# Kernel tuning notes

Hardware: AMD Instinct MI355X
Metric: run time of the kernel (lower is better)

Reference implementation:

```python
import jax, jax.numpy as jnp
import numpy as np

B, D, C, P = 1024, 768, 150, 64  # batch, in_feats, num_labels, proj2 dim
POS_M, NEG_M = 0.7, 1.4


def setup_inputs() -> dict:
    key = jax.random.key(0)
    ks = jax.random.split(key, 8)
    return {
        "x": jax.random.normal(ks[0], (B, D), jnp.float32),
        "lb": jax.random.randint(ks[1], (B,), 0, C + 1),
        "mem": jax.random.normal(ks[2], (C, D), jnp.float32),
        "fc_w": jax.random.normal(ks[3], (2 * D, 2 * D), jnp.float32) * 0.02,
        "fc_b": jnp.zeros((2 * D,), jnp.float32),
        "p1_w": jax.random.normal(ks[4], (1, 2 * D), jnp.float32) * 0.02,
        "p1_b": jnp.zeros((1,), jnp.float32),
        "p2_w": jax.random.normal(ks[5], (P, 2 * D), jnp.float32) * 0.02,
        "p2_b": jnp.zeros((P,), jnp.float32),
    }


def reference(x, lb, mem, fc_w, fc_b, p1_w, p1_b, p2_w, p2_b):
    d = x.shape[1]
    # cat([a, b], 1) @ fc_w.T == a @ Wx.T + b @ Wm.T  (exact split of the linear)
    Wx, Wm = fc_w[:, :d], fc_w[:, d:]
    xh = x @ Wx.T + fc_b                                # [B, 2D]

    # --- get_logit ---
    seen_h = jax.nn.relu(xh[:, None, :] + mem @ Wm.T)   # [B, C, 2D]
    seen = jnp.einsum('bce,e->bc', seen_h, p1_w[0]) + p1_b[0]   # [B, C]
    uh = jax.nn.relu(xh)                                # cat([x, zeros]) path
    unseen = uh @ p1_w.T + p1_b                         # [B, 1]
    logits = jnp.concatenate([seen, unseen], axis=1)    # [B, C+1]

    # --- masked log-softmax losses (pos_adapte) ---
    labels = jax.nn.one_hot(lb, C + 1, dtype=jnp.float32)
    th = jnp.zeros_like(labels).at[:, -1].set(1.0)
    labels = labels.at[:, -1].set(0.0)
    p_mask = labels + th
    n_mask = 1.0 - labels
    BIG = 1e30
    loss1 = -(jax.nn.log_softmax(logits - (1.0 - p_mask) * BIG, -1) * labels).sum(1)
    loss2 = -(jax.nn.log_softmax(logits - (1.0 - n_mask) * BIG, -1) * th).sum(1)
    loss_cls = (loss1 + loss2).mean()

    # --- metric loss on unseen embedding ---
    u = uh @ p2_w.T + p2_b                              # [B, 64]
    u = u / jnp.maximum(jnp.linalg.norm(u, axis=1, keepdims=True), 1e-12)
    sq_n = (u * u).sum(1)
    sq = sq_n[:, None] + sq_n[None, :] - 2.0 * (u @ u.T)
    err = sq <= 0.0
    dist = jnp.sqrt(jnp.clip(sq, 1e-16, None)) * (~err).astype(u.dtype)
    same = lb[:, None] == lb[None, :]
    eye = jnp.eye(dist.shape[0], dtype=bool)
    pos = (same & ~eye).astype(dist.dtype)
    neg = (~same).astype(dist.dtype)
    pos_l = (jax.nn.relu(dist - POS_M) * pos).sum() / jnp.maximum(pos.sum(), 1.0)
    neg_l = (jax.nn.relu(NEG_M - dist) * neg).sum() / jnp.maximum(neg.sum(), 1.0)

    return loss_cls + pos_l + neg_l
```

## Files before the change

### kernel.cpp

```cpp
#include <hip/hip_runtime.h>
#include <math.h>

#define B_    1024
#define D_    768
#define C_    150
#define P_    64
#define TWOD  1536
#define NCLS  151
#define CPAD  256

#define ECHUNKS 16
#define ECHUNK  96

#define ASTR  40
#define USTRU 120
#define USTR  72

#define OFF_MH      0
#define OFF_XH      (OFF_MH + (C_ * TWOD) / 2)
#define OFF_PARTIAL (OFF_XH + (B_ * TWOD) / 2)
#define OFF_UHF     (OFF_PARTIAL + ECHUNKS * B_ * CPAD)
#define OFF_SQN     (OFF_UHF + (B_ * P_) / 2)
#define OFF_CLS     (OFF_SQN + B_)
#define OFF_PAIR    (OFF_CLS + B_)
#define OFF_XBF     (OFF_PAIR + 1024)
#define OFF_MEMBF   (OFF_XBF + (B_ * D_) / 2)
#define OFF_WBF     (OFF_MEMBF + (C_ * D_) / 2)
#define OFF_P2H     (OFF_WBF + (TWOD * TWOD) / 2)
#define OFF_P1H     (OFF_P2H + (P_ * TWOD) / 2)

typedef __bf16    bfx8   __attribute__((ext_vector_type(8)));
typedef _Float16  fp16x8 __attribute__((ext_vector_type(8)));
typedef _Float16  h2v    __attribute__((ext_vector_type(2)));
typedef float     f32x4  __attribute__((ext_vector_type(4)));

__device__ inline ushort f2bf(float f) {
    union { float f; unsigned u; } c; c.f = f;
    unsigned r = c.u + 0x7fffu + ((c.u >> 16) & 1u);
    return (ushort)(r >> 16);
}
__device__ inline ushort f2h(float f) {
    _Float16 h = (_Float16)f;
    return __builtin_bit_cast(ushort, h);
}
__device__ inline unsigned addrelu2(unsigned a, unsigned m) {
    h2v s = __builtin_bit_cast(h2v, a) + __builtin_bit_cast(h2v, m);
    h2v z = {(_Float16)0.f, (_Float16)0.f};
    s = __builtin_elementwise_max(s, z);
    return __builtin_bit_cast(unsigned, s);
}
__device__ inline unsigned relu2(unsigned a) {
    h2v s = __builtin_bit_cast(h2v, a);
    h2v z = {(_Float16)0.f, (_Float16)0.f};
    s = __builtin_elementwise_max(s, z);
    return __builtin_bit_cast(unsigned, s);
}
__device__ inline float dot2acc(unsigned a, unsigned b, float c) {
    return __builtin_amdgcn_fdot2(__builtin_bit_cast(h2v, a),
                                  __builtin_bit_cast(h2v, b), c, false);
}

#define X4   (B_ * D_ / 4)
#define MEM4 (C_ * D_ / 4)
#define W4   (TWOD * TWOD / 4)
#define P24  (P_ * TWOD / 4)
#define P14  (TWOD / 4)
#define TOT4 (X4 + MEM4 + W4 + P24 + P14)

__global__ __launch_bounds__(256) void prep_cvt(
    const float* __restrict__ x, const float* __restrict__ mem,
    const float* __restrict__ w, const float* __restrict__ p2w,
    const float* __restrict__ p1w,
    ushort* __restrict__ xb, ushort* __restrict__ memb,
    ushort* __restrict__ wb, ushort* __restrict__ p2h,
    ushort* __restrict__ p1h)
{
    int i = blockIdx.x * 256 + threadIdx.x;
    if (i >= TOT4) return;
    const float* src; ushort* dst; int off; bool bf;
    if (i < X4)                        { src = x;   dst = xb;   off = i; bf = true; }
    else if (i < X4 + MEM4)            { src = mem; dst = memb; off = i - X4; bf = true; }
    else if (i < X4 + MEM4 + W4)       { src = w;   dst = wb;   off = i - X4 - MEM4; bf = true; }
    else if (i < X4 + MEM4 + W4 + P24) { src = p2w; dst = p2h;  off = i - X4 - MEM4 - W4; bf = false; }
    else                               { src = p1w; dst = p1h;  off = i - X4 - MEM4 - W4 - P24; bf = false; }
    float4 v = ((const float4*)src)[off];
    ushort4 o;
    if (bf) { o.x = f2bf(v.x); o.y = f2bf(v.y); o.z = f2bf(v.z); o.w = f2bf(v.w); }
    else    { o.x = f2h(v.x);  o.y = f2h(v.y);  o.z = f2h(v.z);  o.w = f2h(v.w); }
    ((ushort4*)dst)[off] = o;
}

__global__ __launch_bounds__(256) void gemm_all(
    const ushort* __restrict__ xbf, const ushort* __restrict__ membf,
    const ushort* __restrict__ wbf, const float* __restrict__ fc_b,
    ushort* __restrict__ xh, ushort* __restrict__ mh)
{
    __shared__ ushort As[64 * ASTR];
    __shared__ ushort Bs[128 * ASTR];
    const int id = blockIdx.x;
    const int t  = threadIdx.x;

    const ushort* A; ushort* Out; int M, m0, n0, koff; bool xblk;
    if (id < 192) {
        xblk = true;  A = xbf;  Out = xh; M = B_;
        m0 = (id & 15) * 64; n0 = (id >> 4) * 128; koff = 0;
    } else {
        int q = id - 192;
        xblk = false; A = membf; Out = mh; M = C_;
        m0 = (q % 3) * 64; n0 = (q / 3) * 128; koff = D_;
    }

    const int wave = t >> 6, lane = t & 63;
    const int wm = (wave & 1) * 32, wn = (wave >> 1) * 64;
    const int fm = lane & 15, quad = lane >> 4;

    const int row_a = t >> 2, qa = (t & 3) * 8;
    const int ar = min(m0 + row_a, M - 1);
    const ushort* Arow = A + (size_t)ar * D_ + qa;
    const ushort* Brow = wbf + (size_t)(n0 + row_a) * TWOD + koff + qa;

    f32x4 acc[2][4];
#pragma unroll
    for (int j = 0; j < 4; ++j) {
        float bv = xblk ? fc_b[n0 + wn + j * 16 + fm] : 0.f;
#pragma unroll
        for (int i = 0; i < 2; ++i)
            acc[i][j] = (f32x4){bv, bv, bv, bv};
    }

    uint4 pa  = *(const uint4*)(Arow);
    uint4 pb0 = *(const uint4*)(Brow);
    uint4 pb1 = *(const uint4*)(Brow + 64 * TWOD);

    for (int k0 = 0; k0 < D_; k0 += 32) {
        __syncthreads();
        *(uint4*)&As[row_a * ASTR + qa] = pa;
        *(uint4*)&Bs[row_a * ASTR + qa] = pb0;
        *(uint4*)&Bs[(64 + row_a) * ASTR + qa] = pb1;
        __syncthreads();
        if (k0 + 32 < D_) {
            pa  = *(const uint4*)(Arow + k0 + 32);
            pb0 = *(const uint4*)(Brow + k0 + 32);
            pb1 = *(const uint4*)(Brow + 64 * TWOD + k0 + 32);
        }
        bfx8 af[2], bf[4];
#pragma unroll
        for (int i = 0; i < 2; ++i)
            af[i] = *(const bfx8*)&As[(wm + i * 16 + fm) * ASTR + quad * 8];
#pragma unroll
        for (int j = 0; j < 4; ++j)
            bf[j] = *(const bfx8*)&Bs[(wn + j * 16 + fm) * ASTR + quad * 8];
#pragma unroll
        for (int i = 0; i < 2; ++i)
#pragma unroll
            for (int j = 0; j < 4; ++j)
                acc[i][j] = __builtin_amdgcn_mfma_f32_16x16x32_bf16(
                    af[i], bf[j], acc[i][j], 0, 0, 0);
    }

#pragma unroll
    for (int i = 0; i < 2; ++i)
#pragma unroll
        for (int j = 0; j < 4; ++j)
#pragma unroll
            for (int r = 0; r < 4; ++r) {
                int row = m0 + wm + i * 16 + quad * 4 + r;
                int col = n0 + wn + j * 16 + fm;
                if (row < M) Out[(size_t)row * TWOD + col] = f2h(acc[i][j][r]);
            }
}

__global__ __launch_bounds__(256) void fused_tile(
    const ushort* __restrict__ xh, const ushort* __restrict__ mh,
    const ushort* __restrict__ p1h, const ushort* __restrict__ p2h,
    float* __restrict__ partial)
{
    __shared__ __align__(16) char smem[46080];
    const int t  = threadIdx.x;
    const int b0 = blockIdx.x * 128;
    const int z  = blockIdx.z;
    const int e0 = z * ECHUNK;

    if (blockIdx.y == 3) {
        ushort* Au = (ushort*)smem;
        ushort* Wu = (ushort*)(smem + 30720);
        const int wave = t >> 6, lane = t & 63;
        const int fm = lane & 15, quad = lane >> 4;

        {
            const int row = t >> 1, kh = (t & 1) * 48;
            const ushort* src = xh + (size_t)(b0 + row) * TWOD + e0 + kh;
            uint4 v[6];
#pragma unroll
            for (int i = 0; i < 6; ++i) v[i] = *(const uint4*)&src[i * 8];
#pragma unroll
            for (int i = 0; i < 6; ++i) {
                v[i].x = relu2(v[i].x); v[i].y = relu2(v[i].y);
                v[i].z = relu2(v[i].z); v[i].w = relu2(v[i].w);
                *(uint4*)&Au[row * USTRU + kh + i * 8] = v[i];
            }
        }
        {
            const int row = t >> 2, ks = (t & 3) * 24;
            const ushort* pw = p2h + (size_t)row * TWOD + e0 + ks;
#pragma unroll
            for (int i = 0; i < 3; ++i)
                *(uint4*)&Wu[row * USTRU + ks + i * 8] = *(const uint4*)&pw[i * 8];
        }
        __syncthreads();

        f32x4 uacc[2][4];
#pragma unroll
        for (int i = 0; i < 2; ++i)
#pragma unroll
            for (int j = 0; j < 4; ++j) uacc[i][j] = (f32x4){0.f, 0.f, 0.f, 0.f};
#pragma unroll
        for (int k0 = 0; k0 < ECHUNK; k0 += 32) {
            fp16x8 af[2], bf[4];
#pragma unroll
            for (int i = 0; i < 2; ++i)
                af[i] = *(const fp16x8*)&Au[(wave * 32 + i * 16 + fm) * USTRU + k0 + quad * 8];
#pragma unroll
            for (int j = 0; j < 4; ++j)
                bf[j] = *(const fp16x8*)&Wu[(j * 16 + fm) * USTRU + k0 + quad * 8];
#pragma unroll
            for (int i = 0; i < 2; ++i)
#pragma unroll
                for (int j = 0; j < 4; ++j)
                    uacc[i][j] = __builtin_amdgcn_mfma_f32_16x16x32_f16(
                        af[i], bf[j], uacc[i][j], 0, 0, 0);
        }
#pragma unroll
        for (int i = 0; i < 2; ++i)
#pragma unroll
            for (int j = 0; j < 4; ++j)
#pragma unroll
                for (int r = 0; r < 4; ++r) {
                    int row = b0 + wave * 32 + i * 16 + quad * 4 + r;
                    partial[((size_t)z * B_ + row) * CPAD + 192 + j * 16 + fm] =
                        uacc[i][j][r];
                }
        return;
    }

    unsigned* xT = (unsigned*)smem;
    unsigned* mT = (unsigned*)(smem + 24576);
    unsigned* wT = (unsigned*)(smem + 36864);
    const int c0 = blockIdx.y * 64;
    const int tm = t & 15, tn = t >> 4;

    {
        const int row = t >> 1, ph = (t & 1) * 48;
        const ushort* src = xh + (size_t)(b0 + row) * TWOD + e0 + ph;
        uint4 v[6];
#pragma unroll
        for (int i = 0; i < 6; ++i) v[i] = *(const uint4*)&src[i * 8];
#pragma unroll
        for (int i = 0; i < 6; ++i) {
            const int ep = (t & 1) * 24 + i * 4;
            xT[(ep + 0) * 128 + row] = v[i].x;
            xT[(ep + 1) * 128 + row] = v[i].y;
            xT[(ep + 2) * 128 + row] = v[i].z;
            xT[(ep + 3) * 128 + row] = v[i].w;
        }
    }
    {
        const int col = t & 63, seg = t >> 6;
        const int gc  = c0 + col;
        uint4 v[3];
        if (gc < C_) {
            const ushort* src = mh + (size_t)gc * TWOD + e0 + seg * 24;
#pragma unroll
            for (int i = 0; i < 3; ++i) v[i] = *(const uint4*)&src[i * 8];
        } else {
#pragma unroll
            for (int i = 0; i < 3; ++i) v[i] = make_uint4(0, 0, 0, 0);
        }
#pragma unroll
        for (int i = 0; i < 3; ++i) {
            const int ep = seg * 12 + i * 4;
            mT[(ep + 0) * 64 + col] = v[i].x;
            mT[(ep + 1) * 64 + col] = v[i].y;
            mT[(ep + 2) * 64 + col] = v[i].z;
            mT[(ep + 3) * 64 + col] = v[i].w;
        }
    }
    if (t < 12) {
        uint4 v = *(const uint4*)&p1h[e0 + t * 8];
        wT[t * 4 + 0] = v.x; wT[t * 4 + 1] = v.y;
        wT[t * 4 + 2] = v.z; wT[t * 4 + 3] = v.w;
    }
    __syncthreads();

    float acc[8][4] = {};
#pragma unroll 4
    for (int ep = 0; ep < 48; ++ep) {
        uint4 a0 = *(const uint4*)&xT[ep * 128 + tm * 8];
        uint4 a1 = *(const uint4*)&xT[ep * 128 + tm * 8 + 4];
        uint4 mj = *(const uint4*)&mT[ep * 64 + tn * 4];
        const unsigned wv = wT[ep];
        const unsigned aa[8] = {a0.x, a0.y, a0.z, a0.w, a1.x, a1.y, a1.z, a1.w};
        const unsigned mm[4] = {mj.x, mj.y, mj.z, mj.w};
#pragma unroll
        for (int i = 0; i < 8; ++i)
#pragma unroll
            for (int j = 0; j < 4; ++j)
                acc[i][j] = dot2acc(addrelu2(aa[i], mm[j]), wv, acc[i][j]);
    }

#pragma unroll
    for (int i = 0; i < 8; ++i) {
        const int gb = b0 + tm * 8 + i;
        float4 v = make_float4(acc[i][0], acc[i][1], acc[i][2], acc[i][3]);
        *(float4*)&partial[((size_t)z * B_ + gb) * CPAD + c0 + tn * 4] = v;
    }
}

__global__ __launch_bounds__(256) void reduce_row(
    const float* __restrict__ partial,
    const float* __restrict__ p1b, const float* __restrict__ p2b,
    const int* __restrict__ lb,
    ushort* __restrict__ uhf, float* __restrict__ sqn,
    float* __restrict__ clsbuf)
{
    const int b = blockIdx.x, t = threadIdx.x;
    float v = 0.f;
#pragma unroll
    for (int z = 0; z < ECHUNKS; ++z)
        v += partial[((size_t)z * B_ + b) * CPAD + t];
    if (t < NCLS)       v += p1b[0];
    else if (t >= 192)  v += p2b[t - 192];

    __shared__ float sval[256];
    sval[t] = v;
    __syncthreads();

    if (t < 64) {
        float uv = sval[192 + t];
        float s = uv * uv;
#pragma unroll
        for (int off = 32; off; off >>= 1) s += __shfl_xor(s, off);
        float inv = 1.f / fmaxf(sqrtf(s), 1e-12f);
        uhf[(size_t)b * P_ + t] = f2h(uv * inv);
        if (t == 0) sqn[b] = s * inv * inv;

        const int l = lb[b];
        float mx = -1e30f;
        for (int j = t; j < NCLS; j += 64)
            if (!(j == l && l < C_)) mx = fmaxf(mx, sval[j]);
#pragma unroll
        for (int off = 32; off; off >>= 1) mx = fmaxf(mx, __shfl_xor(mx, off));
        float se = 0.f;
        for (int j = t; j < NCLS; j += 64)
            if (!(j == l && l < C_)) se += expf(sval[j] - mx);
#pragma unroll
        for (int off = 32; off; off >>= 1) se += __shfl_xor(se, off);

        if (t == 0) {
            float l150  = sval[C_];
            float loss2 = mx + logf(se) - l150;
            float loss1 = 0.f;
            if (l < C_) {
                float a  = sval[l];
                float m2 = fmaxf(a, l150);
                loss1 = m2 - a + logf(expf(a - m2) + expf(l150 - m2));
            }
            clsbuf[b] = loss1 + loss2;
        }
    }
}

__global__ __launch_bounds__(256) void pair_loss(
    const ushort* __restrict__ uhf, const float* __restrict__ sqn,
    const int* __restrict__ lb, float* __restrict__ pairpart)
{
    __shared__ ushort ui_s[64 * USTR];
    __shared__ ushort uj_s[64 * USTR];
    __shared__ float sni[64], snj[64];
    __shared__ int   li[64],  lj[64];
    __shared__ float red[4][4];

    const int t  = threadIdx.x;
    const int i0 = blockIdx.x * 64, j0 = blockIdx.y * 64;

    for (int idx = t; idx < 512; idx += 256) {
        int row = idx >> 3, ch = (idx & 7) * 8;
        *(uint4*)&ui_s[row * USTR + ch] =
            *(const uint4*)&uhf[(size_t)(i0 + row) * P_ + ch];
        *(uint4*)&uj_s[row * USTR + ch] =
            *(const uint4*)&uhf[(size_t)(j0 + row) * P_ + ch];
    }
    if (t < 64)       { sni[t] = sqn[i0 + t]; li[t] = lb[i0 + t]; }
    else if (t < 128) { int q = t - 64; snj[q] = sqn[j0 + q]; lj[q] = lb[j0 + q]; }
    __syncthreads();

    const int wave = t >> 6, lane = t & 63;
    const int n = lane & 15, quad = lane >> 4;
    const int iw = wave * 16;

    const fp16x8 af0 = *(const fp16x8*)&ui_s[(iw + n) * USTR + quad * 8];
    const fp16x8 af1 = *(const fp16x8*)&ui_s[(iw + n) * USTR + quad * 8 + 32];

    f32x4 acc[4];
#pragma unroll
    for (int jt = 0; jt < 4; ++jt) {
        const fp16x8 bf0 = *(const fp16x8*)&uj_s[(jt * 16 + n) * USTR + quad * 8];
        const fp16x8 bf1 = *(const fp16x8*)&uj_s[(jt * 16 + n) * USTR + quad * 8 + 32];
        acc[jt] = __builtin_amdgcn_mfma_f32_16x16x32_f16(
            af0, bf0, (f32x4){0.f, 0.f, 0.f, 0.f}, 0, 0, 0);
        acc[jt] = __builtin_amdgcn_mfma_f32_16x16x32_f16(
            af1, bf1, acc[jt], 0, 0, 0);
    }

    float ps = 0.f, pc = 0.f, ns = 0.f, nc = 0.f;
#pragma unroll
    for (int jt = 0; jt < 4; ++jt)
#pragma unroll
        for (int r = 0; r < 4; ++r) {
            const int il = iw + quad * 4 + r;
            const int jl = jt * 16 + n;
            float sq = sni[il] + snj[jl] - 2.f * acc[jt][r];
            float dist = sq > 0.f ? sqrtf(fmaxf(sq, 1e-16f)) : 0.f;
            bool same = (li[il] == lj[jl]);
            if (same) {
                if (i0 + il != j0 + jl) { ps += fmaxf(dist - 0.7f, 0.f); pc += 1.f; }
            } else {
                ns += fmaxf(1.4f - dist, 0.f); nc += 1.f;
            }
        }

#pragma unroll
    for (int off = 32; off; off >>= 1) {
        ps += __shfl_xor(ps, off); pc += __shfl_xor(pc, off);
        ns += __shfl_xor(ns, off); nc += __shfl_xor(nc, off);
    }
    if (lane == 0) { red[0][wave] = ps; red[1][wave] = pc;
                     red[2][wave] = ns; red[3][wave] = nc; }
    __syncthreads();
    if (t == 0) {
        float4 v;
        v.x = red[0][0] + red[0][1] + red[0][2] + red[0][3];
        v.y = red[1][0] + red[1][1] + red[1][2] + red[1][3];
        v.z = red[2][0] + red[2][1] + red[2][2] + red[2][3];
        v.w = red[3][0] + red[3][1] + red[3][2] + red[3][3];
        *(float4*)&pairpart[(size_t)(blockIdx.y * 16 + blockIdx.x) * 4] = v;
    }
}

__global__ __launch_bounds__(256) void finalize(
    const float* __restrict__ clsbuf, const float* __restrict__ pairpart,
    float* __restrict__ out)
{
    __shared__ float red[5][4];
    const int t = threadIdx.x;
    float c = clsbuf[t] + clsbuf[t + 256] + clsbuf[t + 512] + clsbuf[t + 768];
    float4 pp = *(const float4*)&pairpart[(size_t)t * 4];
    float ps = pp.x, pc = pp.y, ns = pp.z, nc = pp.w;
#pragma unroll
    for (int off = 32; off; off >>= 1) {
        c  += __shfl_xor(c, off);
        ps += __shfl_xor(ps, off); pc += __shfl_xor(pc, off);
        ns += __shfl_xor(ns, off); nc += __shfl_xor(nc, off);
    }
    const int wave = t >> 6, lane = t & 63;
    if (lane == 0) { red[0][wave] = c; red[1][wave] = ps; red[2][wave] = pc;
                     red[3][wave] = ns; red[4][wave] = nc; }
    __syncthreads();
    if (t == 0) {
        float C = 0.f, PS = 0.f, PC = 0.f, NS = 0.f, NC = 0.f;
#pragma unroll
        for (int w = 0; w < 4; ++w) {
            C += red[0][w]; PS += red[1][w]; PC += red[2][w];
            NS += red[3][w]; NC += red[4][w];
        }
        out[0] = C / (float)B_ + PS / fmaxf(PC, 1.f) + NS / fmaxf(NC, 1.f);
    }
}

extern "C" void kernel_launch(void* const* d_in, const int* in_sizes, int n_in,
                              void* d_out, int out_size, void* d_ws, size_t ws_size,
                              hipStream_t stream)
{
    const float* x    = (const float*)d_in[0];
    const int*   lb   = (const int*)d_in[1];
    const float* mem  = (const float*)d_in[2];
    const float* fc_w = (const float*)d_in[3];
    const float* fc_b = (const float*)d_in[4];
    const float* p1w  = (const float*)d_in[5];
    const float* p1b  = (const float*)d_in[6];
    const float* p2w  = (const float*)d_in[7];
    const float* p2b  = (const float*)d_in[8];

    float* ws       = (float*)d_ws;
    ushort* mh      = (ushort*)(ws + OFF_MH);
    ushort* xh      = (ushort*)(ws + OFF_XH);
    float* partials = ws + OFF_PARTIAL;
    ushort* uhf     = (ushort*)(ws + OFF_UHF);
    float* sqn      = ws + OFF_SQN;
    float* clsbuf   = ws + OFF_CLS;
    float* pairpart = ws + OFF_PAIR;
    ushort* xbf     = (ushort*)(ws + OFF_XBF);
    ushort* membf   = (ushort*)(ws + OFF_MEMBF);
    ushort* wbf     = (ushort*)(ws + OFF_WBF);
    ushort* p2h     = (ushort*)(ws + OFF_P2H);
    ushort* p1h     = (ushort*)(ws + OFF_P1H);

    prep_cvt<<<(TOT4 + 255) / 256, 256, 0, stream>>>(x, mem, fc_w, p2w, p1w,
                                                     xbf, membf, wbf, p2h, p1h);
    gemm_all<<<228, 256, 0, stream>>>(xbf, membf, wbf, fc_b, xh, mh);
    fused_tile<<<dim3(8, 4, ECHUNKS), 256, 0, stream>>>(xh, mh, p1h, p2h,
                                                        partials);
    reduce_row<<<B_, 256, 0, stream>>>(partials, p1b, p2b, lb, uhf, sqn, clsbuf);
    pair_loss<<<dim3(16, 16), 256, 0, stream>>>(uhf, sqn, lb, pairpart);
    finalize<<<1, 256, 0, stream>>>(clsbuf, pairpart, (float*)d_out);
}
```

Measured before the change: 132.2 us.

## Fuse input precision conversion into GEMM and tile kernels, halve E-chunk count

Removes the separate fp32-to-bf16/fp16 conversion kernel. The GEMM and fused tile kernels now load fp32 inputs directly and convert them in registers before staging to shared memory. The E dimension is split into 8 chunks of 192, processed in two 96-wide phases per block, which halves partial-sum writes and reduction reads. This saves a launch and a full pass over the weights, at the cost of doubled global load bytes in the GEMM and fewer fused_tile blocks.

Result: slower. 144.2 us (+9.1%).

```diff
diff --git a/kernel.cpp b/kernel.cpp
--- a/kernel.cpp
+++ b/kernel.cpp
@@ -9,8 +9,9 @@
 #define NCLS  151
 #define CPAD  256
 
-#define ECHUNKS 16
-#define ECHUNK  96
+#define ECHUNKS 8
+#define ECHUNK  192
+#define EPHASE  96
 
 #define ASTR  40
 #define USTRU 120
@@ -23,11 +24,6 @@
 #define OFF_SQN     (OFF_UHF + (B_ * P_) / 2)
 #define OFF_CLS     (OFF_SQN + B_)
 #define OFF_PAIR    (OFF_CLS + B_)
-#define OFF_XBF     (OFF_PAIR + 1024)
-#define OFF_MEMBF   (OFF_XBF + (B_ * D_) / 2)
-#define OFF_WBF     (OFF_MEMBF + (C_ * D_) / 2)
-#define OFF_P2H     (OFF_WBF + (TWOD * TWOD) / 2)
-#define OFF_P1H     (OFF_P2H + (P_ * TWOD) / 2)
 
 typedef __bf16    bfx8   __attribute__((ext_vector_type(8)));
 typedef _Float16  fp16x8 __attribute__((ext_vector_type(8)));
@@ -42,6 +38,10 @@
 __device__ inline ushort f2h(float f) {
     _Float16 h = (_Float16)f;
     return __builtin_bit_cast(ushort, h);
+}
+__device__ inline unsigned pack2h(float a, float b) {
+    h2v v = {(_Float16)a, (_Float16)b};
+    return __builtin_bit_cast(unsigned, v);
 }
 __device__ inline unsigned addrelu2(unsigned a, unsigned m) {
     h2v s = __builtin_bit_cast(h2v, a) + __builtin_bit_cast(h2v, m);
@@ -59,40 +59,16 @@
     return __builtin_amdgcn_fdot2(__builtin_bit_cast(h2v, a),
                                   __builtin_bit_cast(h2v, b), c, false);
 }
-
-#define X4   (B_ * D_ / 4)
-#define MEM4 (C_ * D_ / 4)
-#define W4   (TWOD * TWOD / 4)
-#define P24  (P_ * TWOD / 4)
-#define P14  (TWOD / 4)
-#define TOT4 (X4 + MEM4 + W4 + P24 + P14)
-
-__global__ __launch_bounds__(256) void prep_cvt(
-    const float* __restrict__ x, const float* __restrict__ mem,
-    const float* __restrict__ w, const float* __restrict__ p2w,
-    const float* __restrict__ p1w,
-    ushort* __restrict__ xb, ushort* __restrict__ memb,
-    ushort* __restrict__ wb, ushort* __restrict__ p2h,
-    ushort* __restrict__ p1h)
-{
-    int i = blockIdx.x * 256 + threadIdx.x;
-    if (i >= TOT4) return;
-    const float* src; ushort* dst; int off; bool bf;
-    if (i < X4)                        { src = x;   dst = xb;   off = i; bf = true; }
-    else if (i < X4 + MEM4)            { src = mem; dst = memb; off = i - X4; bf = true; }
-    else if (i < X4 + MEM4 + W4)       { src = w;   dst = wb;   off = i - X4 - MEM4; bf = true; }
-    else if (i < X4 + MEM4 + W4 + P24) { src = p2w; dst = p2h;  off = i - X4 - MEM4 - W4; bf = false; }
-    else                               { src = p1w; dst = p1h;  off = i - X4 - MEM4 - W4 - P24; bf = false; }
-    float4 v = ((const float4*)src)[off];
-    ushort4 o;
-    if (bf) { o.x = f2bf(v.x); o.y = f2bf(v.y); o.z = f2bf(v.z); o.w = f2bf(v.w); }
-    else    { o.x = f2h(v.x);  o.y = f2h(v.y);  o.z = f2h(v.z);  o.w = f2h(v.w); }
-    ((ushort4*)dst)[off] = o;
+__device__ inline uint4 cvt8bf(float4 a, float4 b) {
+    ushort o[8];
+    o[0] = f2bf(a.x); o[1] = f2bf(a.y); o[2] = f2bf(a.z); o[3] = f2bf(a.w);
+    o[4] = f2bf(b.x); o[5] = f2bf(b.y); o[6] = f2bf(b.z); o[7] = f2bf(b.w);
+    return *(const uint4*)&o[0];
 }
 
 __global__ __launch_bounds__(256) void gemm_all(
-    const ushort* __restrict__ xbf, const ushort* __restrict__ membf,
-    const ushort* __restrict__ wbf, const float* __restrict__ fc_b,
+    const float* __restrict__ xf, const float* __restrict__ memf,
+    const float* __restrict__ fcw, const float* __restrict__ fc_b,
     ushort* __restrict__ xh, ushort* __restrict__ mh)
 {
     __shared__ ushort As[64 * ASTR];
@@ -100,13 +76,13 @@
     const int id = blockIdx.x;
     const int t  = threadIdx.x;
 
-    const ushort* A; ushort* Out; int M, m0, n0, koff; bool xblk;
+    const float* A; ushort* Out; int M, m0, n0, koff; bool xblk;
     if (id < 192) {
-        xblk = true;  A = xbf;  Out = xh; M = B_;
+        xblk = true;  A = xf;   Out = xh; M = B_;
         m0 = (id & 15) * 64; n0 = (id >> 4) * 128; koff = 0;
     } else {
         int q = id - 192;
-        xblk = false; A = membf; Out = mh; M = C_;
+        xblk = false; A = memf; Out = mh; M = C_;
         m0 = (q % 3) * 64; n0 = (q / 3) * 128; koff = D_;
     }
 
@@ -116,8 +92,9 @@
 
     const int row_a = t >> 2, qa = (t & 3) * 8;
     const int ar = min(m0 + row_a, M - 1);
-    const ushort* Arow = A + (size_t)ar * D_ + qa;
-    const ushort* Brow = wbf + (size_t)(n0 + row_a) * TWOD + koff + qa;
+    const float* Arow  = A + (size_t)ar * D_ + qa;
+    const float* Brow0 = fcw + (size_t)(n0 + row_a) * TWOD + koff + qa;
+    const float* Brow1 = Brow0 + (size_t)64 * TWOD;
 
     f32x4 acc[2][4];
 #pragma unroll
@@ -128,20 +105,26 @@
             acc[i][j] = (f32x4){bv, bv, bv, bv};
     }
 
-    uint4 pa  = *(const uint4*)(Arow);
-    uint4 pb0 = *(const uint4*)(Brow);
-    uint4 pb1 = *(const uint4*)(Brow + 64 * TWOD);
+    float4 pa0  = *(const float4*)(Arow),      pa1 = *(const float4*)(Arow + 4);
+    float4 pb00 = *(const float4*)(Brow0),    pb01 = *(const float4*)(Brow0 + 4);
+    float4 pb10 = *(const float4*)(Brow1),    pb11 = *(const float4*)(Brow1 + 4);
 
     for (int k0 = 0; k0 < D_; k0 += 32) {
+        uint4 va  = cvt8bf(pa0, pa1);
+        uint4 vb0 = cvt8bf(pb00, pb01);
+        uint4 vb1 = cvt8bf(pb10, pb11);
         __syncthreads();
-        *(uint4*)&As[row_a * ASTR + qa] = pa;
-        *(uint4*)&Bs[row_a * ASTR + qa] = pb0;
-        *(uint4*)&Bs[(64 + row_a) * ASTR + qa] = pb1;
+        *(uint4*)&As[row_a * ASTR + qa] = va;
+        *(uint4*)&Bs[row_a * ASTR + qa] = vb0;
+        *(uint4*)&Bs[(64 + row_a) * ASTR + qa] = vb1;
         __syncthreads();
         if (k0 + 32 < D_) {
-            pa  = *(const uint4*)(Arow + k0 + 32);
-            pb0 = *(const uint4*)(Brow + k0 + 32);
-            pb1 = *(const uint4*)(Brow + 64 * TWOD + k0 + 32);
+            pa0  = *(const float4*)(Arow + k0 + 32);
+            pa1  = *(const float4*)(Arow + k0 + 36);
+            pb00 = *(const float4*)(Brow0 + k0 + 32);
+            pb01 = *(const float4*)(Brow0 + k0 + 36);
+            pb10 = *(const float4*)(Brow1 + k0 + 32);
+            pb11 = *(const float4*)(Brow1 + k0 + 36);
         }
         bfx8 af[2], bf[4];
 #pragma unroll
@@ -172,7 +155,7 @@
 
 __global__ __launch_bounds__(256) void fused_tile(
     const ushort* __restrict__ xh, const ushort* __restrict__ mh,
-    const ushort* __restrict__ p1h, const ushort* __restrict__ p2h,
+    const float* __restrict__ p1w, const float* __restrict__ p2w,
     float* __restrict__ partial)
 {
     __shared__ __align__(16) char smem[46080];
@@ -187,48 +170,58 @@
         const int wave = t >> 6, lane = t & 63;
         const int fm = lane & 15, quad = lane >> 4;
 
-        {
+        f32x4 uacc[2][4];
+#pragma unroll
+        for (int i = 0; i < 2; ++i)
+#pragma unroll
+            for (int j = 0; j < 4; ++j) uacc[i][j] = (f32x4){0.f, 0.f, 0.f, 0.f};
+
+        for (int ph = 0; ph < 2; ++ph) {
+            const int ep0 = e0 + ph * EPHASE;
             const int row = t >> 1, kh = (t & 1) * 48;
-            const ushort* src = xh + (size_t)(b0 + row) * TWOD + e0 + kh;
+            const ushort* src = xh + (size_t)(b0 + row) * TWOD + ep0 + kh;
             uint4 v[6];
 #pragma unroll
             for (int i = 0; i < 6; ++i) v[i] = *(const uint4*)&src[i * 8];
+            const int prow = t >> 2, ks = (t & 3) * 24;
+            const float* pw = p2w + (size_t)prow * TWOD + ep0 + ks;
+            float4 w[6];
+#pragma unroll
+            for (int i = 0; i < 6; ++i) w[i] = *(const float4*)&pw[i * 4];
+            __syncthreads();
 #pragma unroll
             for (int i = 0; i < 6; ++i) {
                 v[i].x = relu2(v[i].x); v[i].y = relu2(v[i].y);
                 v[i].z = relu2(v[i].z); v[i].w = relu2(v[i].w);
                 *(uint4*)&Au[row * USTRU + kh + i * 8] = v[i];
             }
-        }
-        {
-            const int row = t >> 2, ks = (t & 3) * 24;
-            const ushort* pw = p2h + (size_t)row * TWOD + e0 + ks;
-#pragma unroll
-            for (int i = 0; i < 3; ++i)
-                *(uint4*)&Wu[row * USTRU + ks + i * 8] = *(const uint4*)&pw[i * 8];
-        }
-        __syncthreads();
-
-        f32x4 uacc[2][4];
-#pragma unroll
-        for (int i = 0; i < 2; ++i)
-#pragma unroll
-            for (int j = 0; j < 4; ++j) uacc[i][j] = (f32x4){0.f, 0.f, 0.f, 0.f};
-#pragma unroll
-        for (int k0 = 0; k0 < ECHUNK; k0 += 32) {
-            fp16x8 af[2], bf[4];
-#pragma unroll
-            for (int i = 0; i < 2; ++i)
-                af[i] = *(const fp16x8*)&Au[(wave * 32 + i * 16 + fm) * USTRU + k0 + quad * 8];
-#pragma unroll
-            for (int j = 0; j < 4; ++j)
-                bf[j] = *(const fp16x8*)&Wu[(j * 16 + fm) * USTRU + k0 + quad * 8];
-#pragma unroll
-            for (int i = 0; i < 2; ++i)
+#pragma unroll
+            for (int i = 0; i < 3; ++i) {
+                uint4 o;
+                o.x = pack2h(w[2*i].x, w[2*i].y);
+                o.y = pack2h(w[2*i].z, w[2*i].w);
+                o.z = pack2h(w[2*i+1].x, w[2*i+1].y);
+                o.w = pack2h(w[2*i+1].z, w[2*i+1].w);
+                *(uint4*)&Wu[prow * USTRU + ks + i * 8] = o;
+            }
+            __syncthreads();
+
+#pragma unroll
+            for (int k0 = 0; k0 < EPHASE; k0 += 32) {
+                fp16x8 af[2], bf[4];
+#pragma unroll
+                for (int i = 0; i < 2; ++i)
+                    af[i] = *(const fp16x8*)&Au[(wave * 32 + i * 16 + fm) * USTRU + k0 + quad * 8];
 #pragma unroll
                 for (int j = 0; j < 4; ++j)
-                    uacc[i][j] = __builtin_amdgcn_mfma_f32_16x16x32_f16(
-                        af[i], bf[j], uacc[i][j], 0, 0, 0);
+                    bf[j] = *(const fp16x8*)&Wu[(j * 16 + fm) * USTRU + k0 + quad * 8];
+#pragma unroll
+                for (int i = 0; i < 2; ++i)
+#pragma unroll
+                    for (int j = 0; j < 4; ++j)
+                        uacc[i][j] = __builtin_amdgcn_mfma_f32_16x16x32_f16(
+                            af[i], bf[j], uacc[i][j], 0, 0, 0);
+            }
         }
 #pragma unroll
         for (int i = 0; i < 2; ++i)
@@ -249,12 +242,32 @@
     const int c0 = blockIdx.y * 64;
     const int tm = t & 15, tn = t >> 4;
 
-    {
-        const int row = t >> 1, ph = (t & 1) * 48;
-        const ushort* src = xh + (size_t)(b0 + row) * TWOD + e0 + ph;
+    float acc[8][4] = {};
+
+    for (int ph = 0; ph < 2; ++ph) {
+        const int ep0 = e0 + ph * EPHASE;
+        const int row = t >> 1, phh = (t & 1) * 48;
+        const ushort* src = xh + (size_t)(b0 + row) * TWOD + ep0 + phh;
         uint4 v[6];
 #pragma unroll
         for (int i = 0; i < 6; ++i) v[i] = *(const uint4*)&src[i * 8];
+        const int col = t & 63, seg = t >> 6;
+        const int gc  = c0 + col;
+        uint4 mv[3];
+        if (gc < C_) {
+            const ushort* msrc = mh + (size_t)gc * TWOD + ep0 + seg * 24;
+#pragma unroll
+            for (int i = 0; i < 3; ++i) mv[i] = *(const uint4*)&msrc[i * 8];
+        } else {
+#pragma unroll
+            for (int i = 0; i < 3; ++i) mv[i] = make_uint4(0, 0, 0, 0);
+        }
+        float4 w0, w1;
+        if (t < 12) {
+            w0 = *(const float4*)&p1w[ep0 + t * 8];
+            w1 = *(const float4*)&p1w[ep0 + t * 8 + 4];
+        }
+        __syncthreads();
 #pragma unroll
         for (int i = 0; i < 6; ++i) {
             const int ep = (t & 1) * 24 + i * 4;
@@ -263,49 +276,36 @@
             xT[(ep + 2) * 128 + row] = v[i].z;
             xT[(ep + 3) * 128 + row] = v[i].w;
         }
-    }
-    {
-        const int col = t & 63, seg = t >> 6;
-        const int gc  = c0 + col;
-        uint4 v[3];
-        if (gc < C_) {
-            const ushort* src = mh + (size_t)gc * TWOD + e0 + seg * 24;
-#pragma unroll
-            for (int i = 0; i < 3; ++i) v[i] = *(const uint4*)&src[i * 8];
-        } else {
-#pragma unroll
-            for (int i = 0; i < 3; ++i) v[i] = make_uint4(0, 0, 0, 0);
-        }
 #pragma unroll
         for (int i = 0; i < 3; ++i) {
             const int ep = seg * 12 + i * 4;
-            mT[(ep + 0) * 64 + col] = v[i].x;
-            mT[(ep + 1) * 64 + col] = v[i].y;
-            mT[(ep + 2) * 64 + col] = v[i].z;
-            mT[(ep + 3) * 64 + col] = v[i].w;
-        }
-    }
-    if (t < 12) {
-        uint4 v = *(const uint4*)&p1h[e0 + t * 8];
-        wT[t * 4 + 0] = v.x; wT[t * 4 + 1] = v.y;
-        wT[t * 4 + 2] = v.z; wT[t * 4 + 3] = v.w;
-    }
-    __syncthreads();
-
-    float acc[8][4] = {};
+            mT[(ep + 0) * 64 + col] = mv[i].x;
+            mT[(ep + 1) * 64 + col] = mv[i].y;
+            mT[(ep + 2) * 64 + col] = mv[i].z;
+            mT[(ep + 3) * 64 + col] = mv[i].w;
+        }
+        if (t < 12) {
+            wT[t * 4 + 0] = pack2h(w0.x, w0.y);
+            wT[t * 4 + 1] = pack2h(w0.z, w0.w);
+            wT[t * 4 + 2] = pack2h(w1.x, w1.y);
+            wT[t * 4 + 3] = pack2h(w1.z, w1.w);
+        }
+        __syncthreads();
+
 #pragma unroll 4
-    for (int ep = 0; ep < 48; ++ep) {
-        uint4 a0 = *(const uint4*)&xT[ep * 128 + tm * 8];
-        uint4 a1 = *(const uint4*)&xT[ep * 128 + tm * 8 + 4];
-        uint4 mj = *(const uint4*)&mT[ep * 64 + tn * 4];
-        const unsigned wv = wT[ep];
-        const unsigned aa[8] = {a0.x, a0.y, a0.z, a0.w, a1.x, a1.y, a1.z, a1.w};
-        const unsigned mm[4] = {mj.x, mj.y, mj.z, mj.w};
-#pragma unroll
-        for (int i = 0; i < 8; ++i)
-#pragma unroll
-            for (int j = 0; j < 4; ++j)
-                acc[i][j] = dot2acc(addrelu2(aa[i], mm[j]), wv, acc[i][j]);
+        for (int ep = 0; ep < 48; ++ep) {
+            uint4 a0 = *(const uint4*)&xT[ep * 128 + tm * 8];
+            uint4 a1 = *(const uint4*)&xT[ep * 128 + tm * 8 + 4];
+            uint4 mj = *(const uint4*)&mT[ep * 64 + tn * 4];
+            const unsigned wv = wT[ep];
+            const unsigned aa[8] = {a0.x, a0.y, a0.z, a0.w, a1.x, a1.y, a1.z, a1.w};
+            const unsigned mm[4] = {mj.x, mj.y, mj.z, mj.w};
+#pragma unroll
+            for (int i = 0; i < 8; ++i)
+#pragma unroll
+                for (int j = 0; j < 4; ++j)
+                    acc[i][j] = dot2acc(addrelu2(aa[i], mm[j]), wv, acc[i][j]);
+        }
     }
 
 #pragma unroll
@@ -499,16 +499,9 @@
     float* sqn      = ws + OFF_SQN;
     float* clsbuf   = ws + OFF_CLS;
     float* pairpart = ws + OFF_PAIR;
-    ushort* xbf     = (ushort*)(ws + OFF_XBF);
-    ushort* membf   = (ushort*)(ws + OFF_MEMBF);
-    ushort* wbf     = (ushort*)(ws + OFF_WBF);
-    ushort* p2h     = (ushort*)(ws + OFF_P2H);
-    ushort* p1h     = (ushort*)(ws + OFF_P1H);
-
-    prep_cvt<<<(TOT4 + 255) / 256, 256, 0, stream>>>(x, mem, fc_w, p2w, p1w,
-                                                     xbf, membf, wbf, p2h, p1h);
-    gemm_all<<<228, 256, 0, stream>>>(xbf, membf, wbf, fc_b, xh, mh);
-    fused_tile<<<dim3(8, 4, ECHUNKS), 256, 0, stream>>>(xh, mh, p1h, p2h,
+
+    gemm_all<<<228, 256, 0, stream>>>(x, mem, fc_w, fc_b, xh, mh);
+    fused_tile<<<dim3(8, 4, ECHUNKS), 256, 0, stream>>>(xh, mh, p1w, p2w,
                                                         partials);
     reduce_row<<<B_, 256, 0, stream>>>(partials, p1b, p2b, lb, uhf, sqn, clsbuf);
     pair_loss<<<dim3(16, 16), 256, 0, stream>>>(uhf, sqn, lb, pairpart);
```
